# Performance work log

Measured on AMD Instinct MI355X. Metric: run time of the kernel, lower is better.

## Reference

```python
import jax, jax.numpy as jnp
import numpy as np

OUT_FEATURES = 4096
IN_FEATURES = 4096
RANK = 64
ALPHA = 1.0
SCALING = ALPHA / float(RANK)  # w1 direct, w2 factored -> effective_alpha = alpha


def setup_inputs() -> dict:
    key = jax.random.key(0)
    k_x, k_w1, k_a, k_b = jax.random.split(key, 4)
    x = jax.random.normal(k_x, (4, 2048, IN_FEATURES), dtype=jnp.float32)
    lokr_w1 = jax.random.normal(k_w1, (8, 8), dtype=jnp.float32)        # [out_l, in_m]
    lokr_w2_a = jax.random.normal(k_a, (512, RANK), dtype=jnp.float32)  # [out_k, rank]
    lokr_w2_b = jax.random.normal(k_b, (RANK, 512), dtype=jnp.float32)  # [rank, in_n]
    return {"x": x, "lokr_w1": lokr_w1, "lokr_w2_a": lokr_w2_a, "lokr_w2_b": lokr_w2_b}


def reference(x, lokr_w1, lokr_w2_a, lokr_w2_b):
    # w2 = w2_a @ w2_b : [out_k, in_n]
    w2 = lokr_w2_a @ lokr_w2_b
    # kron(w1, w2): element (i*out_k + k, j*in_n + l) = w1[i,j] * w2[k,l]
    out_l, in_m = lokr_w1.shape
    out_k, in_n = w2.shape
    diff = jnp.einsum('ij,kl->ikjl', lokr_w1, w2).reshape(out_l * out_k, in_m * in_n)
    diff = diff * SCALING  # [out_features, in_features]
    # F.linear(x, diff) = x @ diff.T
    return jnp.einsum('bsi,oi->bso', x, diff)
```

## Files before the change

kernel.cpp:

```cpp
#include <hip/hip_runtime.h>
#include <hip/hip_bf16.h>


typedef __attribute__((ext_vector_type(4))) float f32x4;
typedef __attribute__((ext_vector_type(8))) short s16x8;
typedef __attribute__((ext_vector_type(4))) short s16x4;

__device__ inline unsigned short f2bf(float f) {
    unsigned u = __float_as_uint(f);
    u += 0x7FFF + ((u >> 16) & 1);
    return (unsigned short)(u >> 16);
}

__global__ void lokr_pre(const float* __restrict__ w1,
                         const float* __restrict__ a,
                         const float* __restrict__ b,
                         unsigned short* __restrict__ b_bf,
                         unsigned short* __restrict__ a_bf,
                         float* __restrict__ w1s) {
    int i = blockIdx.x * 256 + threadIdx.x;
    if (i < 32768) {
        b_bf[i] = f2bf(b[i]);
        a_bf[i] = f2bf(a[i]);
    }
    if (i < 64) w1s[i] = w1[i] * (1.0f / 64.0f);
}

#define LSTR 72

__global__ __launch_bounds__(256, 4) void lokr_main(
    const float* __restrict__ x,
    const unsigned short* __restrict__ b_bf,
    const unsigned short* __restrict__ a_bf,
    const float* __restrict__ w1s,
    float* __restrict__ out)
{
    __shared__ __attribute__((aligned(16))) unsigned short xs[2][64 * LSTR];
    __shared__ float w1_s[64];
    unsigned short* vs = &xs[0][0];

    const int t    = threadIdx.x;
    const int wave = t >> 6;
    const int lane = t & 63;
    const int col  = lane & 15;
    const int quad = lane >> 4;
    const long rowbase = (long)blockIdx.x * 64;

    if (t < 64) w1_s[t] = w1s[t];

    const int lrow = t >> 4;
    const int lcol = (t & 15) * 4;

    float4 xb[4];
    {
        const float* xg = x + (rowbase + lrow) * 512 + lcol;
        #pragma unroll
        for (int i = 0; i < 4; ++i)
            xb[i] = *(const float4*)(xg + (long)i * 16 * 512);
    }
    #pragma unroll
    for (int i = 0; i < 4; ++i) {
        s16x4 h;
        h[0] = (short)f2bf(xb[i].x); h[1] = (short)f2bf(xb[i].y);
        h[2] = (short)f2bf(xb[i].z); h[3] = (short)f2bf(xb[i].w);
        *(s16x4*)&xs[0][(lrow + i * 16) * LSTR + lcol] = h;
    }
    __syncthreads();

    f32x4 acc[4];
    #pragma unroll
    for (int m = 0; m < 4; ++m) acc[m] = (f32x4){0.f, 0.f, 0.f, 0.f};

    const unsigned short* brow = b_bf + (wave * 16 + col) * 512 + quad * 8;
    s16x8 bc0 = *(const s16x8*)(brow);
    s16x8 bc1 = *(const s16x8*)(brow + 32);

    #pragma unroll 2
    for (int s = 0; s < 8; ++s) {
        s16x8 bn0, bn1;
        if (s < 7) {
            bn0 = *(const s16x8*)(brow + (s + 1) * 64);
            bn1 = *(const s16x8*)(brow + (s + 1) * 64 + 32);
            const float* xg = x + (rowbase + lrow) * 512 + (s + 1) * 64 + lcol;
            #pragma unroll
            for (int i = 0; i < 4; ++i)
                xb[i] = *(const float4*)(xg + (long)i * 16 * 512);
        }
        const unsigned short* xa = &xs[s & 1][col * LSTR + quad * 8];
        #pragma unroll
        for (int m = 0; m < 4; ++m) {
            s16x8 a0 = *(const s16x8*)(xa + m * 16 * LSTR);
            s16x8 a1 = *(const s16x8*)(xa + m * 16 * LSTR + 32);
            acc[m] = __builtin_amdgcn_mfma_f32_16x16x32_bf16(a0, bc0, acc[m], 0, 0, 0);
            acc[m] = __builtin_amdgcn_mfma_f32_16x16x32_bf16(a1, bc1, acc[m], 0, 0, 0);
        }
        if (s < 7) {
            #pragma unroll
            for (int i = 0; i < 4; ++i) {
                s16x4 h;
                h[0] = (short)f2bf(xb[i].x); h[1] = (short)f2bf(xb[i].y);
                h[2] = (short)f2bf(xb[i].z); h[3] = (short)f2bf(xb[i].w);
                *(s16x4*)&xs[(s + 1) & 1][(lrow + i * 16) * LSTR + lcol] = h;
            }
            __syncthreads();
            bc0 = bn0; bc1 = bn1;
        }
    }

    #pragma unroll
    for (int m = 0; m < 4; ++m) {
        float own[4], oth[4], tij[8];
        #pragma unroll
        for (int j = 0; j < 4; ++j) own[j] = acc[m][j];
        #pragma unroll
        for (int j = 0; j < 4; ++j) oth[j] = __shfl_xor(own[j], 16);
        if ((quad & 1) == 0) {
            #pragma unroll
            for (int j = 0; j < 4; ++j) { tij[j] = own[j]; tij[4 + j] = oth[j]; }
        } else {
            #pragma unroll
            for (int j = 0; j < 4; ++j) { tij[j] = oth[j]; tij[4 + j] = own[j]; }
        }
        const int plocal = m * 2 + (quad >> 1);
        const int oib = (quad & 1) * 4;
        #pragma unroll
        for (int oo = 0; oo < 4; ++oo) {
            float v = 0.f;
            #pragma unroll
            for (int j = 0; j < 8; ++j) v += w1_s[(oib + oo) * 8 + j] * tij[j];
            vs[(plocal * 8 + oib + oo) * LSTR + wave * 16 + col] = f2bf(v);
        }
    }
    __syncthreads();

    s16x8 va0[4], va1[4];
    #pragma unroll
    for (int m = 0; m < 4; ++m) {
        const unsigned short* vp = &vs[(m * 16 + col) * LSTR + quad * 8];
        va0[m] = *(const s16x8*)(vp);
        va1[m] = *(const s16x8*)(vp + 32);
    }

    const unsigned short* ab = a_bf + (wave * 128 + col) * 64 + quad * 8;
    s16x8 ac0 = *(const s16x8*)(ab);
    s16x8 ac1 = *(const s16x8*)(ab + 32);

    float* ob = out + (rowbase + col) * 512 + wave * 128 + quad * 4;

    for (int nt = 0; nt < 8; ++nt) {
        s16x8 an0, an1;
        if (nt < 7) {
            an0 = *(const s16x8*)(ab + (nt + 1) * 1024);
            an1 = *(const s16x8*)(ab + (nt + 1) * 1024 + 32);
        }
        #pragma unroll
        for (int m = 0; m < 4; ++m) {
            f32x4 c = {0.f, 0.f, 0.f, 0.f};
            c = __builtin_amdgcn_mfma_f32_16x16x32_bf16(ac0, va0[m], c, 0, 0, 0);
            c = __builtin_amdgcn_mfma_f32_16x16x32_bf16(ac1, va1[m], c, 0, 0, 0);
            *(f32x4*)(ob + (long)m * 16 * 512 + nt * 16) = c;
        }
        if (nt < 7) { ac0 = an0; ac1 = an1; }
    }
}

extern "C" void kernel_launch(void* const* d_in, const int* in_sizes, int n_in,
                              void* d_out, int out_size, void* d_ws, size_t ws_size,
                              hipStream_t stream) {
    const float* x  = (const float*)d_in[0];
    const float* w1 = (const float*)d_in[1];
    const float* a  = (const float*)d_in[2];
    const float* b  = (const float*)d_in[3];

    unsigned short* b_bf = (unsigned short*)d_ws;
    unsigned short* a_bf = b_bf + 32768;
    float*          w1s  = (float*)(a_bf + 32768);

    lokr_pre<<<128, 256, 0, stream>>>(w1, a, b, b_bf, a_bf, w1s);
    lokr_main<<<1024, 256, 0, stream>>>(x, b_bf, a_bf, w1s, (float*)d_out);
}
```

Before: 256.9 us.

## Load x fragments directly into MFMA registers and shrink blocks to two waves

Removes the shared-memory staging and double-buffered barriers for x in the first GEMM; each wave now loads its own 16-row x fragments from global memory, converts them to bf16 in registers and feeds the MFMAs directly. Blocks drop to 128 threads covering 32 rows, with each wave computing all 64 rank columns and later 256 output columns. This removes LDS traffic and syncs but makes each wave fetch the full B factor and hold more fragment registers.

New measurement: 260.0 us. No clear change (+1.2%).

```diff
diff --git a/kernel.cpp b/kernel.cpp
--- a/kernel.cpp
+++ b/kernel.cpp
@@ -4,12 +4,20 @@
 
 typedef __attribute__((ext_vector_type(4))) float f32x4;
 typedef __attribute__((ext_vector_type(8))) short s16x8;
-typedef __attribute__((ext_vector_type(4))) short s16x4;
 
 __device__ inline unsigned short f2bf(float f) {
     unsigned u = __float_as_uint(f);
     u += 0x7FFF + ((u >> 16) & 1);
     return (unsigned short)(u >> 16);
+}
+
+__device__ inline s16x8 pack8(float4 lo, float4 hi) {
+    s16x8 h;
+    h[0] = (short)f2bf(lo.x); h[1] = (short)f2bf(lo.y);
+    h[2] = (short)f2bf(lo.z); h[3] = (short)f2bf(lo.w);
+    h[4] = (short)f2bf(hi.x); h[5] = (short)f2bf(hi.y);
+    h[6] = (short)f2bf(hi.z); h[7] = (short)f2bf(hi.w);
+    return h;
 }
 
 __global__ void lokr_pre(const float* __restrict__ w1,
@@ -28,90 +36,83 @@
 
 #define LSTR 72
 
-__global__ __launch_bounds__(256, 4) void lokr_main(
+__global__ __launch_bounds__(128, 4) void lokr_main(
     const float* __restrict__ x,
     const unsigned short* __restrict__ b_bf,
     const unsigned short* __restrict__ a_bf,
     const float* __restrict__ w1s,
     float* __restrict__ out)
 {
-    __shared__ __attribute__((aligned(16))) unsigned short xs[2][64 * LSTR];
+    __shared__ __attribute__((aligned(16))) unsigned short vs[32 * LSTR];
     __shared__ float w1_s[64];
-    unsigned short* vs = &xs[0][0];
 
     const int t    = threadIdx.x;
     const int wave = t >> 6;
     const int lane = t & 63;
     const int col  = lane & 15;
     const int quad = lane >> 4;
-    const long rowbase = (long)blockIdx.x * 64;
+    const long rowbase = (long)blockIdx.x * 32;
+    const long wrow    = rowbase + wave * 16;
 
-    if (t < 64) w1_s[t] = w1s[t];
+    w1_s[lane] = w1s[lane];
 
-    const int lrow = t >> 4;
-    const int lcol = (t & 15) * 4;
-
-    float4 xb[4];
-    {
-        const float* xg = x + (rowbase + lrow) * 512 + lcol;
-        #pragma unroll
-        for (int i = 0; i < 4; ++i)
-            xb[i] = *(const float4*)(xg + (long)i * 16 * 512);
-    }
-    #pragma unroll
-    for (int i = 0; i < 4; ++i) {
-        s16x4 h;
-        h[0] = (short)f2bf(xb[i].x); h[1] = (short)f2bf(xb[i].y);
-        h[2] = (short)f2bf(xb[i].z); h[3] = (short)f2bf(xb[i].w);
-        *(s16x4*)&xs[0][(lrow + i * 16) * LSTR + lcol] = h;
-    }
-    __syncthreads();
+    const float* xw = x + (wrow + col) * 512 + quad * 8;
+    const unsigned short* bw = b_bf + col * 512 + quad * 8;
 
     f32x4 acc[4];
     #pragma unroll
-    for (int m = 0; m < 4; ++m) acc[m] = (f32x4){0.f, 0.f, 0.f, 0.f};
+    for (int rt = 0; rt < 4; ++rt) acc[rt] = (f32x4){0.f, 0.f, 0.f, 0.f};
 
-    const unsigned short* brow = b_bf + (wave * 16 + col) * 512 + quad * 8;
-    s16x8 bc0 = *(const s16x8*)(brow);
-    s16x8 bc1 = *(const s16x8*)(brow + 32);
+    float4 xb[4];
+    xb[0] = *(const float4*)(xw);
+    xb[1] = *(const float4*)(xw + 4);
+    xb[2] = *(const float4*)(xw + 32);
+    xb[3] = *(const float4*)(xw + 36);
+
+    s16x8 bc[4][2];
+    #pragma unroll
+    for (int rt = 0; rt < 4; ++rt) {
+        bc[rt][0] = *(const s16x8*)(bw + rt * 8192);
+        bc[rt][1] = *(const s16x8*)(bw + rt * 8192 + 32);
+    }
 
     #pragma unroll 2
     for (int s = 0; s < 8; ++s) {
-        s16x8 bn0, bn1;
+        s16x8 a0 = pack8(xb[0], xb[1]);
+        s16x8 a1 = pack8(xb[2], xb[3]);
+        s16x8 bn[4][2];
         if (s < 7) {
-            bn0 = *(const s16x8*)(brow + (s + 1) * 64);
-            bn1 = *(const s16x8*)(brow + (s + 1) * 64 + 32);
-            const float* xg = x + (rowbase + lrow) * 512 + (s + 1) * 64 + lcol;
             #pragma unroll
-            for (int i = 0; i < 4; ++i)
-                xb[i] = *(const float4*)(xg + (long)i * 16 * 512);
+            for (int rt = 0; rt < 4; ++rt) {
+                bn[rt][0] = *(const s16x8*)(bw + rt * 8192 + (s + 1) * 64);
+                bn[rt][1] = *(const s16x8*)(bw + rt * 8192 + (s + 1) * 64 + 32);
+            }
+            const float* xg = xw + (s + 1) * 64;
+            xb[0] = *(const float4*)(xg);
+            xb[1] = *(const float4*)(xg + 4);
+            xb[2] = *(const float4*)(xg + 32);
+            xb[3] = *(const float4*)(xg + 36);
         }
-        const unsigned short* xa = &xs[s & 1][col * LSTR + quad * 8];
         #pragma unroll
-        for (int m = 0; m < 4; ++m) {
-            s16x8 a0 = *(const s16x8*)(xa + m * 16 * LSTR);
-            s16x8 a1 = *(const s16x8*)(xa + m * 16 * LSTR + 32);
-            acc[m] = __builtin_amdgcn_mfma_f32_16x16x32_bf16(a0, bc0, acc[m], 0, 0, 0);
-            acc[m] = __builtin_amdgcn_mfma_f32_16x16x32_bf16(a1, bc1, acc[m], 0, 0, 0);
+        for (int rt = 0; rt < 4; ++rt) {
+            acc[rt] = __builtin_amdgcn_mfma_f32_16x16x32_bf16(a0, bc[rt][0], acc[rt], 0, 0, 0);
+            acc[rt] = __builtin_amdgcn_mfma_f32_16x16x32_bf16(a1, bc[rt][1], acc[rt], 0, 0, 0);
         }
         if (s < 7) {
             #pragma unroll
-            for (int i = 0; i < 4; ++i) {
-                s16x4 h;
-                h[0] = (short)f2bf(xb[i].x); h[1] = (short)f2bf(xb[i].y);
-                h[2] = (short)f2bf(xb[i].z); h[3] = (short)f2bf(xb[i].w);
-                *(s16x4*)&xs[(s + 1) & 1][(lrow + i * 16) * LSTR + lcol] = h;
+            for (int rt = 0; rt < 4; ++rt) {
+                bc[rt][0] = bn[rt][0]; bc[rt][1] = bn[rt][1];
             }
-            __syncthreads();
-            bc0 = bn0; bc1 = bn1;
         }
     }
 
+    const int p   = quad >> 1;
+    const int oib = (quad & 1) * 4;
     #pragma unroll
-    for (int m = 0; m < 4; ++m) {
+    for (int rt = 0; rt < 4; ++rt) {
         float own[4], oth[4], tij[8];
         #pragma unroll
-        for (int j = 0; j < 4; ++j) own[j] = acc[m][j];
+        for (int j = 0; j < 4; ++j) own[j] = acc[rt][j];
         #pragma unroll
         for (int j = 0; j < 4; ++j) oth[j] = __shfl_xor(own[j], 16);
         if ((quad & 1) == 0) {
@@ -121,46 +122,44 @@
             #pragma unroll
             for (int j = 0; j < 4; ++j) { tij[j] = oth[j]; tij[4 + j] = own[j]; }
         }
-        const int plocal = m * 2 + (quad >> 1);
-        const int oib = (quad & 1) * 4;
         #pragma unroll
         for (int oo = 0; oo < 4; ++oo) {
             float v = 0.f;
             #pragma unroll
             for (int j = 0; j < 8; ++j) v += w1_s[(oib + oo) * 8 + j] * tij[j];
-            vs[(plocal * 8 + oib + oo) * LSTR + wave * 16 + col] = f2bf(v);
+            vs[(wave * 16 + p * 8 + oib + oo) * LSTR + rt * 16 + col] = f2bf(v);
         }
     }
     __syncthreads();
 
-    s16x8 va0[4], va1[4];
+    s16x8 va[2][2];
     #pragma unroll
-    for (int m = 0; m < 4; ++m) {
+    for (int m = 0; m < 2; ++m) {
         const unsigned short* vp = &vs[(m * 16 + col) * LSTR + quad * 8];
-        va0[m] = *(const s16x8*)(vp);
-        va1[m] = *(const s16x8*)(vp + 32);
+        va[m][0] = *(const s16x8*)(vp);
+        va[m][1] = *(const s16x8*)(vp + 32);
     }
 
-    const unsigned short* ab = a_bf + (wave * 128 + col) * 64 + quad * 8;
+    const unsigned short* ab = a_bf + (wave * 256 + col) * 64 + quad * 8;
     s16x8 ac0 = *(const s16x8*)(ab);
     s16x8 ac1 = *(const s16x8*)(ab + 32);
 
-    float* ob = out + (rowbase + col) * 512 + wave * 128 + quad * 4;
+    float* ob = out + (rowbase + col) * 512 + wave * 256 + quad * 4;
 
-    for (int nt = 0; nt < 8; ++nt) {
+    for (int nt = 0; nt < 16; ++nt) {
         s16x8 an0, an1;
-        if (nt < 7) {
+        if (nt < 15) {
             an0 = *(const s16x8*)(ab + (nt + 1) * 1024);
             an1 = *(const s16x8*)(ab + (nt + 1) * 1024 + 32);
         }
         #pragma unroll
-        for (int m = 0; m < 4; ++m) {
+        for (int m = 0; m < 2; ++m) {
             f32x4 c = {0.f, 0.f, 0.f, 0.f};
-            c = __builtin_amdgcn_mfma_f32_16x16x32_bf16(ac0, va0[m], c, 0, 0, 0);
-            c = __builtin_amdgcn_mfma_f32_16x16x32_bf16(ac1, va1[m], c, 0, 0, 0);
+            c = __builtin_amdgcn_mfma_f32_16x16x32_bf16(ac0, va[m][0], c, 0, 0, 0);
+            c = __builtin_amdgcn_mfma_f32_16x16x32_bf16(ac1, va[m][1], c, 0, 0, 0);
             *(f32x4*)(ob + (long)m * 16 * 512 + nt * 16) = c;
         }
-        if (nt < 7) { ac0 = an0; ac1 = an1; }
+        if (nt < 15) { ac0 = an0; ac1 = an1; }
     }
 }
 
@@ -177,5 +176,5 @@
     float*          w1s  = (float*)(a_bf + 32768);
 
     lokr_pre<<<128, 256, 0, stream>>>(w1, a, b, b_bf, a_bf, w1s);
-    lokr_main<<<1024, 256, 0, stream>>>(x, b_bf, a_bf, w1s, (float*)d_out);
+    lokr_main<<<2048, 128, 0, stream>>>(x, b_bf, a_bf, w1s, (float*)d_out);
 }
```
